# Optimization experiments

Measured on AMD Instinct MI355X. Metric: run time of the kernel, lower is better.

## Reference

```python
import jax, jax.numpy as jnp
import numpy as np

N_QUBITS = 12
DIM = 2 ** N_QUBITS
BATCH = 2048


def setup_inputs() -> dict:
    key = jax.random.key(0)
    k1, k2, k3 = jax.random.split(key, 3)
    inputs = jax.random.normal(k1, (BATCH, N_QUBITS), dtype=jnp.float32)
    weight = jax.random.normal(k2, (3 + 2 * N_QUBITS,), dtype=jnp.float32)
    entangle_matrix = jax.random.normal(k3, (DIM, DIM), dtype=jnp.float32)
    return {"inputs": inputs, "weight": weight, "entangle_matrix": entangle_matrix}


def _encode(ry_angles, rz_angles):
    # Encoder: state = prod over qubits of first column of (Rz*Ry) per qubit.
    ry = ry_angles / 2
    rz = rz_angles / 2
    a = jnp.cos(ry) * jnp.exp(-1j * rz)  # entry11 (row bit = 0)
    b = jnp.sin(ry) * jnp.exp(1j * rz)   # entry21 (row bit = 1)
    col2 = jnp.stack([a, b], axis=-1).astype(jnp.complex64)  # [B, n, 2]
    B, n = ry.shape
    v = jnp.ones((B, 1), dtype=jnp.complex64)
    for q in range(n):  # Kronecker fold over qubits (big-endian, matches dec2bin)
        v = (v[:, :, None] * col2[:, q][:, None, :]).reshape(B, -1)
    return v  # [B, 2^n]


def _rot_mat(w):
    # rot_mat: per-qubit Rx(w[q]) @ Rz(w[n+q]), then full Kronecker product.
    n = w.shape[0] // 2
    tx = (w[:n] / 2).astype(jnp.complex64)
    tz = (w[n:] / 2).astype(jnp.complex64)
    c, s = jnp.cos(tx), jnp.sin(tx)
    rx = jnp.stack([jnp.stack([c, -1j * s], -1),
                    jnp.stack([-1j * s, c], -1)], -2)  # [n,2,2]
    ez = jnp.exp(-1j * tz)
    zero = jnp.zeros_like(ez)
    rz = jnp.stack([jnp.stack([ez, zero], -1),
                    jnp.stack([zero, jnp.exp(1j * tz)], -1)], -2)  # [n,2,2]
    mats = jnp.einsum('qij,qjk->qik', rx, rz)
    M = mats[0]
    for q in range(1, n):
        M = jnp.kron(M, mats[q])
    return M  # [2^n, 2^n]


def _ry2(theta):
    a = theta / 2
    c, s = jnp.cos(a), jnp.sin(a)
    return jnp.stack([jnp.stack([c, -s]), jnp.stack([s, c])])  # [2,2] real


def _final_rot(th3):
    # final_rot_mat: Rz-form @ Ry-form @ Rx-form (all ry_mat_list), kron with identity.
    rot = _ry2(th3[2]) @ (_ry2(th3[1]) @ _ry2(th3[0]))
    eye = jnp.eye(DIM // 2, dtype=jnp.complex64)
    return jnp.kron(rot.astype(jnp.complex64), eye)  # [DIM, DIM]


def reference(inputs, weight, entangle_matrix):
    # initial=False branch
    ry_angles = inputs
    rz_angles = jnp.square(inputs)
    v = _encode(ry_angles, rz_angles)                 # [B, DIM] complex64
    E = entangle_matrix.astype(jnp.complex64)
    R = _rot_mat(weight[3:])
    M = E @ R @ E                                     # [DIM, DIM]
    v = v @ M.T                                       # tensordot dims ([-1],[-1])
    F = _final_rot(weight[:3])
    v = v @ F.T
    half = DIM // 2
    # vector[:, half:] = 0 then sum |.|^2  <=>  sum over first half
    return jnp.sum(jnp.square(jnp.abs(v[:, :half])), axis=-1)  # [B] float32
```

## Files before the change

### kernel.cpp

```cpp
#include <hip/hip_runtime.h>
#include <math.h>

#define QDIM 4096
#define NQ 12
#define QBATCH 2048

typedef _Float16 f16x8 __attribute__((ext_vector_type(8)));
typedef float f32x4 __attribute__((ext_vector_type(4)));
typedef int i32x4 __attribute__((ext_vector_type(4)));

__device__ __forceinline__ void gld_lds16(const void* gptr, void* ldsptr) {
    __builtin_amdgcn_global_load_lds(
        (const __attribute__((address_space(1))) void*)gptr,
        (__attribute__((address_space(3))) void*)ldsptr,
        16, 0, 0);
}

__device__ __forceinline__ int q8(float x) {
    float y = fminf(fmaxf(x, -127.f), 127.f);
    return (int)rintf(y);
}
__device__ __forceinline__ int pack4_i8(int a, int b, int c, int d) {
    return (a & 0xFF) | ((b & 0xFF) << 8) | ((c & 0xFF) << 16) | ((d & 0xFF) << 24);
}

__global__ __launch_bounds__(256) void conv_kernel(
    const float* __restrict__ E, const float* __restrict__ wgt,
    _Float16* __restrict__ Eh, signed char* __restrict__ G8)
{
    float th = 0.5f * (wgt[0] + wgt[1] + wgt[2]);
    float c0 = cosf(th), c1 = -sinf(th);
    const float qs = 127.f / 6.f;
    size_t flat = ((size_t)blockIdx.x * 256 + threadIdx.x) * 8;
    size_t n = flat >> 12;
    size_t k = flat & (QDIM - 1);
    const float* p0 = E + n * QDIM + k;
    const float* p1 = p0 + (size_t)QBATCH * QDIM;
    float4 a0 = ((const float4*)p0)[0], a1 = ((const float4*)p0)[1];
    float4 b0 = ((const float4*)p1)[0], b1 = ((const float4*)p1)[1];
    f16x8 h0 = { (_Float16)a0.x, (_Float16)a0.y, (_Float16)a0.z, (_Float16)a0.w,
                 (_Float16)a1.x, (_Float16)a1.y, (_Float16)a1.z, (_Float16)a1.w };
    f16x8 h1 = { (_Float16)b0.x, (_Float16)b0.y, (_Float16)b0.z, (_Float16)b0.w,
                 (_Float16)b1.x, (_Float16)b1.y, (_Float16)b1.z, (_Float16)b1.w };
    *(f16x8*)&Eh[n * QDIM + k] = h0;
    *(f16x8*)&Eh[(n + QBATCH) * QDIM + k] = h1;
    float g[8] = { c0*a0.x + c1*b0.x, c0*a0.y + c1*b0.y, c0*a0.z + c1*b0.z, c0*a0.w + c1*b0.w,
                   c0*a1.x + c1*b1.x, c0*a1.y + c1*b1.y, c0*a1.z + c1*b1.z, c0*a1.w + c1*b1.w };
    int2 gp = { pack4_i8(q8(g[0]*qs), q8(g[1]*qs), q8(g[2]*qs), q8(g[3]*qs)),
                pack4_i8(q8(g[4]*qs), q8(g[5]*qs), q8(g[6]*qs), q8(g[7]*qs)) };
    *(int2*)&G8[n * QDIM + k] = gp;
}

__global__ __launch_bounds__(256) void expand_kernel(
    const float* __restrict__ inputs, _Float16* __restrict__ A1,
    float* __restrict__ out)
{
    __shared__ float ab[NQ][4];
    const int b = blockIdx.x;
    const int tid = threadIdx.x;
    if (tid == 0) out[b] = 0.f;
    if (tid < NQ) {
        float x = inputs[b * NQ + tid];
        float ry = 0.5f * x;
        float rz = 0.5f * x * x;
        float ca = cosf(ry), sa = sinf(ry), cz = cosf(rz), sz = sinf(rz);
        ab[tid][0] = ca * cz;  ab[tid][1] = -ca * sz;
        ab[tid][2] = sa * cz;  ab[tid][3] =  sa * sz;
    }
    __syncthreads();
    float pr0 = 1.f, pi0 = 0.f;
#pragma unroll
    for (int q = 0; q < 8; ++q) {
        int bit = (tid >> (7 - q)) & 1;
        float cr = ab[q][bit * 2 + 0], ci = ab[q][bit * 2 + 1];
        float nr = pr0 * cr - pi0 * ci;
        float ni = pr0 * ci + pi0 * cr;
        pr0 = nr; pi0 = ni;
    }
    f16x8 vr[2], vi[2];
#pragma unroll
    for (int u = 0; u < 16; ++u) {
        float pr = pr0, pi = pi0;
#pragma unroll
        for (int q = 8; q < 12; ++q) {
            int bit = (u >> (11 - q)) & 1;
            float cr = ab[q][bit * 2 + 0], ci = ab[q][bit * 2 + 1];
            float nr = pr * cr - pi * ci;
            float ni = pr * ci + pi * cr;
            pr = nr; pi = ni;
        }
        vr[u >> 3][u & 7] = (_Float16)pr;
        vi[u >> 3][u & 7] = (_Float16)pi;
    }
    const int idx0 = tid * 16;
    *(f16x8*)&A1[(size_t)b * QDIM + idx0] = vr[0];
    *(f16x8*)&A1[(size_t)b * QDIM + idx0 + 8] = vr[1];
    *(f16x8*)&A1[(size_t)(b + QBATCH) * QDIM + idx0] = vi[0];
    *(f16x8*)&A1[(size_t)(b + QBATCH) * QDIM + idx0 + 8] = vi[1];
}

#define VMCNT(N_) asm volatile("s_waitcnt vmcnt(" #N_ ")" ::: "memory")
#define SBAR()                              \
    do {                                    \
        asm volatile("" ::: "memory");      \
        __builtin_amdgcn_s_barrier();       \
        asm volatile("" ::: "memory");      \
    } while (0)

__global__ __launch_bounds__(512, 2) void gemm_f16_256(
    const _Float16* __restrict__ A, const _Float16* __restrict__ B,
    _Float16* __restrict__ C, int N)
{
    const int K = QDIM;
    __shared__ __attribute__((aligned(16))) _Float16 As[2][256 * 64];
    __shared__ __attribute__((aligned(16))) _Float16 Bs[2][256 * 64];

    const int tid  = threadIdx.x;
    const int wave = tid >> 6;
    const int lane = tid & 63;
    const int bm0 = blockIdx.y * 256;
    const int bn0 = blockIdx.x * 256;
    const int wm0 = (wave >> 2) * 128;
    const int wn0 = (wave & 3) * 64;
    const int q = lane >> 4;
    const int r = lane & 15;
    const int rx = r & 7;

    f32x4 acc[8][4];
#pragma unroll
    for (int i = 0; i < 8; ++i)
#pragma unroll
        for (int j = 0; j < 4; ++j) acc[i][j] = (f32x4){0.f, 0.f, 0.f, 0.f};

    const int srow = tid >> 3;
    const int scol = ((tid & 7) ^ (srow & 7)) * 8;
    const _Float16* gA = A + (size_t)(bm0 + srow) * K + scol;
    const _Float16* gB = B + (size_t)(bn0 + srow) * K + scol;

#define STG_A(D, KK, NN) gld_lds16(gA + (size_t)(NN) * 64 * K + (KK), &As[D][(NN) * 4096 + wave * 512])
#define STG_B(D, KK, NN) gld_lds16(gB + (size_t)(NN) * 64 * K + (KK), &Bs[D][(NN) * 4096 + wave * 512])

#define RD_A4(DST, D, IB)                                                          \
    _Pragma("unroll")                                                              \
    for (int ii = 0; ii < 4; ++ii) {                                               \
        _Pragma("unroll")                                                          \
        for (int ss = 0; ss < 2; ++ss)                                             \
            DST[ii][ss] = *(const f16x8*)&As[D][(wm0 + ((IB) + ii) * 16 + r) * 64  \
                                                + (((ss * 4 + q) ^ rx) * 8)];      \
    }
#define RD_B2(DST, D, JB)                                                          \
    _Pragma("unroll")                                                              \
    for (int jj = 0; jj < 2; ++jj) {                                               \
        _Pragma("unroll")                                                          \
        for (int ss = 0; ss < 2; ++ss)                                             \
            DST[jj][ss] = *(const f16x8*)&Bs[D][(wn0 + ((JB) + jj) * 16 + r) * 64  \
                                                + (((ss * 4 + q) ^ rx) * 8)];      \
    }
#define MM8(AR, BR, I0, J0)                                                        \
    _Pragma("unroll")                                                              \
    for (int ii = 0; ii < 4; ++ii) {                                               \
        _Pragma("unroll")                                                          \
        for (int jj = 0; jj < 2; ++jj) {                                           \
            acc[(I0) + ii][(J0) + jj] = __builtin_amdgcn_mfma_f32_16x16x32_f16(    \
                AR[ii][0], BR[jj][0], acc[(I0) + ii][(J0) + jj], 0, 0, 0);         \
            acc[(I0) + ii][(J0) + jj] = __builtin_amdgcn_mfma_f32_16x16x32_f16(    \
                AR[ii][1], BR[jj][1], acc[(I0) + ii][(J0) + jj], 0, 0, 0);         \
        }                                                                          \
    }

    f16x8 a0[4][2], a1[4][2], b0[2][2], b1[2][2];

    STG_B(0, 0, 0); STG_B(0, 0, 1); STG_B(0, 0, 2); STG_B(0, 0, 3);
    STG_A(0, 0, 0); STG_A(0, 0, 2); STG_A(0, 0, 1); STG_A(0, 0, 3);
    VMCNT(0);
    SBAR();
    RD_A4(a0, 0, 0);
    RD_B2(b0, 0, 0);

    for (int t = 0; t < 64; ++t) {
        const int d = t & 1;
        const int e = d ^ 1;
        const int kn = ((t + 1) & 63) * 64;

        STG_B(e, kn, 0); STG_B(e, kn, 1);
        VMCNT(2);
        RD_B2(b1, d, 2);
        SBAR();
        __builtin_amdgcn_s_setprio(1);
        MM8(a0, b0, 0, 0);
        __builtin_amdgcn_s_setprio(0);
        SBAR();

        STG_B(e, kn, 2); STG_B(e, kn, 3);
        RD_A4(a1, d, 4);
        SBAR();
        __builtin_amdgcn_s_setprio(1);
        MM8(a0, b1, 0, 2);
        __builtin_amdgcn_s_setprio(0);
        SBAR();

        STG_A(e, kn, 0); STG_A(e, kn, 2);
        SBAR();
        __builtin_amdgcn_s_setprio(1);
        MM8(a1, b1, 4, 2);
        __builtin_amdgcn_s_setprio(0);
        SBAR();

        STG_A(e, kn, 1); STG_A(e, kn, 3);
        VMCNT(2);
        SBAR();
        __builtin_amdgcn_s_setprio(1);
        MM8(a1, b0, 4, 0);
        __builtin_amdgcn_s_setprio(0);
        RD_A4(a0, e, 0);
        RD_B2(b0, e, 0);
        SBAR();
    }

#pragma unroll
    for (int i = 0; i < 8; ++i) {
        const int crow = bm0 + wm0 + i * 16 + q * 4;
#pragma unroll
        for (int rr = 0; rr < 4; ++rr)
#pragma unroll
            for (int j = 0; j < 4; ++j)
                C[(size_t)(crow + rr) * N + bn0 + wn0 + j * 16 + r] = (_Float16)acc[i][j][rr];
    }
#undef STG_A
#undef STG_B
#undef RD_A4
#undef RD_B2
#undef MM8
}

__global__ __launch_bounds__(256) void butterfly_kernel(
    const _Float16* __restrict__ u1, const float* __restrict__ wgt,
    signed char* __restrict__ A2, float* __restrict__ scaleA)
{
    __shared__ float sRe[4366];
    __shared__ float sIm[4366];
    __shared__ float mats[NQ][8];
    __shared__ float red[8];
    const int blk = blockIdx.x;
    const int tid = threadIdx.x;
    const int ah = tid >> 4;
    const int al = tid & 15;

    if (tid < NQ) {
        float tx = 0.5f * wgt[3 + tid];
        float tz = 0.5f * wgt[15 + tid];
        float c = cosf(tx), s = sinf(tx), cz = cosf(tz), sz = sinf(tz);
        mats[tid][0] =  c * cz;  mats[tid][1] = -c * sz;
        mats[tid][2] =  s * sz;  mats[tid][3] = -s * cz;
        mats[tid][4] = -s * sz;  mats[tid][5] = -s * cz;
        mats[tid][6] =  c * cz;  mats[tid][7] =  c * sz;
    }

    float xr[16], xi[16];
    {
        const _Float16* pRe = u1 + (size_t)blk * QDIM + tid * 16;
        const _Float16* pIm = u1 + (size_t)(blk + QBATCH) * QDIM + tid * 16;
        f16x8 r0 = ((const f16x8*)pRe)[0], r1 = ((const f16x8*)pRe)[1];
        f16x8 i0 = ((const f16x8*)pIm)[0], i1 = ((const f16x8*)pIm)[1];
#pragma unroll
        for (int j = 0; j < 8; ++j) {
            xr[j] = (float)r0[j]; xr[8 + j] = (float)r1[j];
            xi[j] = (float)i0[j]; xi[8 + j] = (float)i1[j];
        }
    }
    __syncthreads();

#define BFLY_STAGE(arrR, arrI, K_, Q_)                                         \
    {                                                                          \
        const float m00r = mats[Q_][0], m00i = mats[Q_][1];                    \
        const float m01r = mats[Q_][2], m01i = mats[Q_][3];                    \
        const float m10r = mats[Q_][4], m10i = mats[Q_][5];                    \
        const float m11r = mats[Q_][6], m11i = mats[Q_][7];                    \
        _Pragma("unroll")                                                      \
        for (int t = 0; t < 8; ++t) {                                          \
            int i0 = ((t >> (K_)) << ((K_) + 1)) | (t & ((1 << (K_)) - 1));    \
            int i1 = i0 | (1 << (K_));                                         \
            float x0r = arrR[i0], x0i = arrI[i0];                              \
            float x1r = arrR[i1], x1i = arrI[i1];                              \
            arrR[i0] = m00r * x0r - m00i * x0i + m01r * x1r - m01i * x1i;      \
            arrI[i0] = m00r * x0i + m00i * x0r + m01r * x1i + m01i * x1r;      \
            arrR[i1] = m10r * x0r - m10i * x0i + m11r * x1r - m11i * x1i;      \
            arrI[i1] = m10r * x0i + m10i * x0r + m11r * x1i + m11i * x1r;      \
        }                                                                      \
    }

#pragma unroll
    for (int p = 0; p < 4; ++p) BFLY_STAGE(xr, xi, p, 11 - p);

#pragma unroll
    for (int c = 0; c < 16; ++c) {
        sRe[273 * ah + 17 * al + c] = xr[c];
        sIm[273 * ah + 17 * al + c] = xi[c];
    }
    __syncthreads();

    float yr[16], yi[16];
#pragma unroll
    for (int b = 0; b < 16; ++b) {
        yr[b] = sRe[273 * ah + 17 * b + al];
        yi[b] = sIm[273 * ah + 17 * b + al];
    }
#pragma unroll
    for (int p = 0; p < 4; ++p) BFLY_STAGE(yr, yi, p, 7 - p);

#pragma unroll
    for (int b = 0; b < 16; ++b) {
        sRe[273 * ah + 17 * b + al] = yr[b];
        sIm[273 * ah + 17 * b + al] = yi[b];
    }
    __syncthreads();

    float zr[16], zi[16];
#pragma unroll
    for (int a = 0; a < 16; ++a) {
        zr[a] = sRe[273 * a + 17 * ah + al];
        zi[a] = sIm[273 * a + 17 * ah + al];
    }
#pragma unroll
    for (int p = 0; p < 4; ++p) BFLY_STAGE(zr, zi, p, 3 - p);

    float mR = 0.f, mI = 0.f;
#pragma unroll
    for (int j = 0; j < 16; ++j) {
        mR = fmaxf(mR, fabsf(zr[j]));
        mI = fmaxf(mI, fabsf(zi[j]));
    }
#pragma unroll
    for (int off = 32; off > 0; off >>= 1) {
        mR = fmaxf(mR, __shfl_xor(mR, off, 64));
        mI = fmaxf(mI, __shfl_xor(mI, off, 64));
    }
    const int wid = tid >> 6;
    if ((tid & 63) == 0) { red[wid] = mR; red[4 + wid] = mI; }
    __syncthreads();
    mR = fmaxf(fmaxf(red[0], red[1]), fmaxf(red[2], red[3]));
    mI = fmaxf(fmaxf(red[4], red[5]), fmaxf(red[6], red[7]));
    mR = fmaxf(mR, 1e-30f);
    mI = fmaxf(mI, 1e-30f);
    if (tid == 0) {
        scaleA[blk] = mR / 127.f;
        scaleA[blk + QBATCH] = mI / 127.f;
    }
    const float invR = 127.f / mR, invI = 127.f / mI;

    signed char* oRe = A2 + (size_t)blk * QDIM + ah * 16 + al;
    signed char* oIm = A2 + (size_t)(blk + QBATCH) * QDIM + ah * 16 + al;
#pragma unroll
    for (int a = 0; a < 16; ++a) {
        oRe[a * 256] = (signed char)q8(zr[a] * invR);
        oIm[a * 256] = (signed char)q8(zi[a] * invI);
    }
#undef BFLY_STAGE
}

__global__ __launch_bounds__(256) void gemm2_i8(
    const signed char* __restrict__ A, const signed char* __restrict__ B,
    const float* __restrict__ scaleA, float* __restrict__ out)
{
    const int K = QDIM;
    __shared__ __attribute__((aligned(16))) signed char As[128 * 128];
    __shared__ __attribute__((aligned(16))) signed char Bs[128 * 128];

    const int tid  = threadIdx.x;
    const int wave = tid >> 6;
    const int lane = tid & 63;
    const int bn0 = blockIdx.x * 128;
    const int bm0 = blockIdx.y * 128;
    const int wm = (wave >> 1) * 64;
    const int wn = (wave & 1) * 64;
    const int q = lane >> 4;
    const int r = lane & 15;
    const int rx = r & 7;

    i32x4 acc[4][4];
#pragma unroll
    for (int i = 0; i < 4; ++i)
#pragma unroll
        for (int j = 0; j < 4; ++j) acc[i][j] = (i32x4){0, 0, 0, 0};

    const signed char* gA[4];
    const signed char* gB[4];
    char* lA[4];
    char* lB[4];
#pragma unroll
    for (int n = 0; n < 4; ++n) {
        int c = n * 256 + tid;
        int row = c >> 3;
        int gcol = (c & 7) ^ (row & 7);
        gA[n] = A + (size_t)(bm0 + row) * K + gcol * 16;
        gB[n] = B + (size_t)(bn0 + row) * K + gcol * 16;
        lA[n] = (char*)As + (n * 256 + wave * 64) * 16;
        lB[n] = (char*)Bs + (n * 256 + wave * 64) * 16;
    }

    for (int kk = 0; kk < K; kk += 128) {
#pragma unroll
        for (int n = 0; n < 4; ++n) {
            gld_lds16(gA[n] + kk, lA[n]);
            gld_lds16(gB[n] + kk, lB[n]);
        }
        __syncthreads();

#pragma unroll
        for (int s = 0; s < 2; ++s) {
            i32x4 af[4], bf[4];
#pragma unroll
            for (int i = 0; i < 4; ++i) {
                int row = wm + i * 16 + r;
                af[i] = *(const i32x4*)&As[row * 128 + (((s * 4 + q) ^ rx) * 16)];
            }
#pragma unroll
            for (int j = 0; j < 4; ++j) {
                int row = wn + j * 16 + r;
                bf[j] = *(const i32x4*)&Bs[row * 128 + (((s * 4 + q) ^ rx) * 16)];
            }
#pragma unroll
            for (int i = 0; i < 4; ++i)
#pragma unroll
                for (int j = 0; j < 4; ++j)
                    acc[i][j] = __builtin_amdgcn_mfma_i32_16x16x64_i8(af[i], bf[j], acc[i][j], 0, 0, 0);
        }
        __syncthreads();
    }

    const float dqG = 6.f / 127.f;
#pragma unroll
    for (int i = 0; i < 4; ++i) {
#pragma unroll
        for (int rr = 0; rr < 4; ++rr) {
            const int row = bm0 + wm + i * 16 + q * 4 + rr;
            const float sc = scaleA[row] * dqG;
            float v = 0.f;
#pragma unroll
            for (int j = 0; j < 4; ++j) {
                float t = sc * (float)acc[i][j][rr];
                v = fmaf(t, t, v);
            }
            v += __shfl_xor(v, 1, 64);
            v += __shfl_xor(v, 2, 64);
            v += __shfl_xor(v, 4, 64);
            v += __shfl_xor(v, 8, 64);
            if (r == 0) atomicAdd(&out[row & (QBATCH - 1)], v);
        }
    }
}

extern "C" void kernel_launch(void* const* d_in, const int* in_sizes, int n_in,
                              void* d_out, int out_size, void* d_ws, size_t ws_size,
                              hipStream_t stream)
{
    const float* inputs = (const float*)d_in[0];
    const float* weight = (const float*)d_in[1];
    const float* E      = (const float*)d_in[2];
    float* out = (float*)d_out;

    char* ws = (char*)d_ws;
    const size_t MB = 1024 * 1024;
    _Float16*    Eh     = (_Float16*)   (ws + 0);
    signed char* G8     = (signed char*)(ws + 32 * MB);
    _Float16*    A1     = (_Float16*)   (ws + 40 * MB);
    _Float16*    u1     = (_Float16*)   (ws + 72 * MB);
    signed char* A2     = (signed char*)(ws + 104 * MB);
    float*       scaleA = (float*)      (ws + 120 * MB);

    conv_kernel<<<(QBATCH * QDIM / 8) / 256, 256, 0, stream>>>(E, weight, Eh, G8);
    expand_kernel<<<QBATCH, 256, 0, stream>>>(inputs, A1, out);
    gemm_f16_256<<<dim3(QDIM / 256, QDIM / 256), 512, 0, stream>>>(A1, Eh, u1, QDIM);
    butterfly_kernel<<<QBATCH, 256, 0, stream>>>(u1, weight, A2, scaleA);
    gemm2_i8<<<dim3(2048 / 128, QDIM / 128), 256, 0, stream>>>(A2, G8, scaleA, out);
}
```

Baseline: 318.6 us.

## Restructure f16 GEMM main loop into staggered A/B prefetch pipeline

Rewrites the GEMM K-loop to process two K-tiles per iteration with explicit buffer indices. B for the next tile is prefetched a full tile ahead, while A is streamed into the other buffer half-by-half as it is consumed. Explicit lgkmcnt waits are added so LDS reads complete before the MFMAs. The aim is deeper overlap of global-to-LDS loads with MFMA compute, at the cost of more complex buffer hazards and extra barriers/waits.

Measured after the change: 299.0 us. -6.1%, faster.

```diff
diff --git a/kernel.cpp b/kernel.cpp
--- a/kernel.cpp
+++ b/kernel.cpp
@@ -100,6 +100,8 @@
 }
 
 #define VMCNT(N_) asm volatile("s_waitcnt vmcnt(" #N_ ")" ::: "memory")
+#define LGKM0()   asm volatile("s_waitcnt lgkmcnt(0)" ::: "memory")
+#define LGKM8()   asm volatile("s_waitcnt lgkmcnt(8)" ::: "memory")
 #define SBAR()                              \
     do {                                    \
         asm volatile("" ::: "memory");      \
@@ -139,6 +141,8 @@
 
 #define STG_A(D, KK, NN) gld_lds16(gA + (size_t)(NN) * 64 * K + (KK), &As[D][(NN) * 4096 + wave * 512])
 #define STG_B(D, KK, NN) gld_lds16(gB + (size_t)(NN) * 64 * K + (KK), &Bs[D][(NN) * 4096 + wave * 512])
+#define STG_AH(D, KK, H) do { STG_A(D, KK, 2*(H)); STG_A(D, KK, 2*(H)+1); } while (0)
+#define STG_BH(D, KK, H) do { STG_B(D, KK, 2*(H)); STG_B(D, KK, 2*(H)+1); } while (0)
 
 #define RD_A4(DST, D, IB)                                                          \
     _Pragma("unroll")                                                              \
@@ -170,52 +174,84 @@
 
     f16x8 a0[4][2], a1[4][2], b0[2][2], b1[2][2];
 
-    STG_B(0, 0, 0); STG_B(0, 0, 1); STG_B(0, 0, 2); STG_B(0, 0, 3);
-    STG_A(0, 0, 0); STG_A(0, 0, 2); STG_A(0, 0, 1); STG_A(0, 0, 3);
+    STG_AH(0, 0, 0); STG_AH(0, 0, 1);
+    STG_BH(0, 0, 0); STG_BH(0, 0, 1);
+    STG_BH(1, 64, 0); STG_BH(1, 64, 1);
+    VMCNT(4);
+    SBAR();
+
+    for (int tau = 0; tau < 32; ++tau) {
+        const int k1 = (2 * tau + 1) * 64;
+        const int k2 = ((2 * tau + 2) & 63) * 64;
+        const int k3 = ((2 * tau + 3) & 63) * 64;
+
+        RD_A4(a0, 0, 0); RD_B2(b0, 0, 0);
+        STG_AH(1, k1, 0);
+        LGKM8();
+        SBAR(); LGKM0();
+        __builtin_amdgcn_s_setprio(1);
+        MM8(a0, b0, 0, 0);
+        __builtin_amdgcn_s_setprio(0);
+        SBAR();
+
+        RD_B2(b1, 0, 2);
+        STG_AH(1, k1, 1);
+        SBAR(); LGKM0();
+        __builtin_amdgcn_s_setprio(1);
+        MM8(a0, b1, 0, 2);
+        __builtin_amdgcn_s_setprio(0);
+        SBAR();
+
+        RD_A4(a1, 0, 4);
+        STG_BH(0, k2, 0);
+        SBAR(); LGKM0();
+        __builtin_amdgcn_s_setprio(1);
+        MM8(a1, b1, 4, 2);
+        __builtin_amdgcn_s_setprio(0);
+        SBAR();
+
+        STG_BH(0, k2, 1);
+        VMCNT(4);
+        SBAR(); LGKM0();
+        __builtin_amdgcn_s_setprio(1);
+        MM8(a1, b0, 4, 0);
+        __builtin_amdgcn_s_setprio(0);
+        SBAR();
+
+        RD_A4(a0, 1, 0); RD_B2(b0, 1, 0);
+        STG_AH(0, k2, 0);
+        LGKM8();
+        SBAR(); LGKM0();
+        __builtin_amdgcn_s_setprio(1);
+        MM8(a0, b0, 0, 0);
+        __builtin_amdgcn_s_setprio(0);
+        SBAR();
+
+        RD_B2(b1, 1, 2);
+        STG_AH(0, k2, 1);
+        SBAR(); LGKM0();
+        __builtin_amdgcn_s_setprio(1);
+        MM8(a0, b1, 0, 2);
+        __builtin_amdgcn_s_setprio(0);
+        SBAR();
+
+        RD_A4(a1, 1, 4);
+        STG_BH(1, k3, 0);
+        SBAR(); LGKM0();
+        __builtin_amdgcn_s_setprio(1);
+        MM8(a1, b1, 4, 2);
+        __builtin_amdgcn_s_setprio(0);
+        SBAR();
+
+        STG_BH(1, k3, 1);
+        VMCNT(4);
+        SBAR(); LGKM0();
+        __builtin_amdgcn_s_setprio(1);
+        MM8(a1, b0, 4, 0);
+        __builtin_amdgcn_s_setprio(0);
+        SBAR();
+    }
     VMCNT(0);
-    SBAR();
-    RD_A4(a0, 0, 0);
-    RD_B2(b0, 0, 0);
-
-    for (int t = 0; t < 64; ++t) {
-        const int d = t & 1;
-        const int e = d ^ 1;
-        const int kn = ((t + 1) & 63) * 64;
-
-        STG_B(e, kn, 0); STG_B(e, kn, 1);
-        VMCNT(2);
-        RD_B2(b1, d, 2);
-        SBAR();
-        __builtin_amdgcn_s_setprio(1);
-        MM8(a0, b0, 0, 0);
-        __builtin_amdgcn_s_setprio(0);
-        SBAR();
-
-        STG_B(e, kn, 2); STG_B(e, kn, 3);
-        RD_A4(a1, d, 4);
-        SBAR();
-        __builtin_amdgcn_s_setprio(1);
-        MM8(a0, b1, 0, 2);
-        __builtin_amdgcn_s_setprio(0);
-        SBAR();
-
-        STG_A(e, kn, 0); STG_A(e, kn, 2);
-        SBAR();
-        __builtin_amdgcn_s_setprio(1);
-        MM8(a1, b1, 4, 2);
-        __builtin_amdgcn_s_setprio(0);
-        SBAR();
-
-        STG_A(e, kn, 1); STG_A(e, kn, 3);
-        VMCNT(2);
-        SBAR();
-        __builtin_amdgcn_s_setprio(1);
-        MM8(a1, b0, 4, 0);
-        __builtin_amdgcn_s_setprio(0);
-        RD_A4(a0, e, 0);
-        RD_B2(b0, e, 0);
-        SBAR();
-    }
 
 #pragma unroll
     for (int i = 0; i < 8; ++i) {
@@ -228,6 +264,8 @@
     }
 #undef STG_A
 #undef STG_B
+#undef STG_AH
+#undef STG_BH
 #undef RD_A4
 #undef RD_B2
 #undef MM8
```
